# Kernel tuning notes

Measured on AMD Instinct MI355X. Metric: run time of the kernel, lower is better.

Reference implementation:

```python
import jax, jax.numpy as jnp
import numpy as np

B, S, F = 4, 2048, 512
H, DH, OUT = 8, 64, 512  # attention_dim=512 -> head_dim=64
NEG_SLOPE = 0.01


def setup_inputs() -> dict:
    key = jax.random.key(0)
    ks = jax.random.split(key, 9)
    sc_in = 1.0 / np.sqrt(F)
    sc_hd = 1.0 / np.sqrt(H * DH)
    return {
        "x": jax.random.normal(ks[0], (B, S, F), dtype=jnp.float32),
        "Wq": jax.random.normal(ks[1], (F, H, DH), dtype=jnp.float32) * sc_in,
        "bq": jnp.zeros((H, DH), dtype=jnp.float32),
        "Wk": jax.random.normal(ks[2], (F, H, DH), dtype=jnp.float32) * sc_in,
        "bk": jnp.zeros((H, DH), dtype=jnp.float32),
        "Wv": jax.random.normal(ks[3], (F, H, DH), dtype=jnp.float32) * sc_in,
        "bv": jnp.zeros((H, DH), dtype=jnp.float32),
        "Wo": jax.random.normal(ks[4], (H, DH, OUT), dtype=jnp.float32) * sc_hd,
        "bo": jnp.zeros((OUT,), dtype=jnp.float32),
    }


def reference(x, Wq, bq, Wk, bk, Wv, bv, Wo, bo):
    # QKV projections: DenseGeneral(axis=-1, features=(H, DH)) -> [B, S, H, DH]
    q = jnp.einsum('bsf,fhd->bshd', x, Wq) + bq
    k = jnp.einsum('bsf,fhd->bshd', x, Wk) + bk
    v = jnp.einsum('bsf,fhd->bshd', x, Wv) + bv

    # Pairwise squared L2: l2[b,h,i,j] = ||q[b,i,h]-k[b,j,h]||^2
    q2 = jnp.sum(q * q, axis=-1)              # [B, S, H]
    k2 = jnp.sum(k * k, axis=-1)              # [B, S, H]
    qk = jnp.einsum('bihd,bjhd->bhij', q, k)  # [B, H, S, S]
    l2 = (q2.transpose(0, 2, 1)[:, :, :, None]
          + k2.transpose(0, 2, 1)[:, :, None, :]
          - 2.0 * qk)

    # softmax over key axis j, then weights.T @ value (note the transpose:
    # output token index is j, summed over query index i, as in the original)
    w = jax.nn.softmax(-l2, axis=-1)                  # [B, H, Si, Sj]
    attn = jnp.einsum('bhij,bihd->bjhd', w, v)        # [B, S, H, DH]

    # out DenseGeneral contracting (H, DH)
    out = jnp.einsum('bshd,hdo->bso', attn, Wo) + bo
    return jnp.where(out >= 0, out, NEG_SLOPE * out)
```

## Files before the change

### kernel.cpp

```cpp
#include <hip/hip_runtime.h>


typedef __attribute__((ext_vector_type(8))) short bf16x8;
typedef __attribute__((ext_vector_type(4))) float f32x4;
typedef __attribute__((ext_vector_type(4))) unsigned short u16x4;

#define MFMA16 __builtin_amdgcn_mfma_f32_16x16x32_bf16
#define LOG2E 1.4426950408889634f
#define TWO_LOG2E 2.8853900817779268f

__device__ inline unsigned short f2bf(float f) {
  unsigned int u = __float_as_uint(f);
  unsigned int r = 0x7fffu + ((u >> 16) & 1u);
  return (unsigned short)((u + r) >> 16);
}
__device__ inline float bf2f(unsigned short h) {
  return __uint_as_float(((unsigned int)h) << 16);
}
__device__ inline float fexp2(float x) { return __builtin_amdgcn_exp2f(x); }

__device__ inline void gl_lds16(const unsigned short* g, unsigned short* lds) {
  __builtin_amdgcn_global_load_lds(
      (const __attribute__((address_space(1))) unsigned int*)g,
      (__attribute__((address_space(3))) unsigned int*)lds, 16, 0, 0);
}

#define NXB4 (8192*512/4)

__global__ __launch_bounds__(256) void prep(
    const float* __restrict__ x, const float* __restrict__ bq,
    const float* __restrict__ bk, const float* __restrict__ bv,
    unsigned short* __restrict__ xb, float* __restrict__ biasp) {
  int i = blockIdx.x * blockDim.x + threadIdx.x;
  if (i < NXB4) {
    f32x4 v = ((const f32x4*)x)[i];
    u16x4 o;
    o.x = f2bf(v.x); o.y = f2bf(v.y); o.z = f2bf(v.z); o.w = f2bf(v.w);
    ((u16x4*)xb)[i] = o;
    return;
  }
  i -= NXB4;
  if (i < 1536) {
    biasp[i] = (i < 512) ? bq[i] : (i < 1024) ? bk[i - 512] : bv[i - 1024];
  }
}

__global__ __launch_bounds__(256) void packW(
    const float* __restrict__ Wq, const float* __restrict__ Wk,
    const float* __restrict__ Wv, const float* __restrict__ Wo,
    unsigned short* __restrict__ wqkvT, unsigned short* __restrict__ woT) {
  const int m = blockIdx.x >> 6;
  const int n0 = ((blockIdx.x >> 3) & 7) * 64;
  const int f0 = (blockIdx.x & 7) * 64;
  const float* W = (m == 0) ? Wq : (m == 1) ? Wk : (m == 2) ? Wv : Wo;
  __shared__ float tile[64][65];
  const int t = threadIdx.x;
  const int c = t & 63, r4 = t >> 6;
#pragma unroll
  for (int k = 0; k < 16; ++k) {
    const int r = r4 + k * 4;
    tile[r][c] = W[(size_t)(f0 + r) * 512 + n0 + c];
  }
  __syncthreads();
#pragma unroll
  for (int k = 0; k < 16; ++k) {
    const int n_idx = r4 + k * 4, f_idx = c;
    const unsigned short v = f2bf(tile[f_idx][n_idx]);
    if (m < 3)
      wqkvT[(size_t)(m * 512 + n0 + n_idx) * 512 + f0 + f_idx] = v;
    else
      woT[(size_t)(n0 + n_idx) * 512 + f0 + f_idx] = v;
  }
}

template<int MODE>
__global__ __launch_bounds__(256) void gemm_bt(
    const unsigned short* __restrict__ A, const unsigned short* __restrict__ Bt,
    const float* __restrict__ bias,
    unsigned short* __restrict__ o_q, unsigned short* __restrict__ o_k,
    unsigned short* __restrict__ o_v, float* __restrict__ o_f,
    float* __restrict__ k2l_g, int K) {
  const int lid = blockIdx.x + blockIdx.y * gridDim.x;
  const int tot = gridDim.x * gridDim.y;
  const int lid2 = (lid & 7) * (tot >> 3) + (lid >> 3);
  const int m0 = (lid2 / gridDim.x) * 128;
  const int n0 = (lid2 % gridDim.x) * 128;
  const int tid = threadIdx.x;
  const int w = tid >> 6, l = tid & 63, lg = l >> 4, ll = l & 15;
  const int wr = w >> 1, wc = w & 1;
  __shared__ unsigned short a_lds[2][128 * 32];
  __shared__ unsigned short b_lds[2][128 * 32];
  f32x4 acc[4][4] = {};
  const int nkt = K >> 5;
  const int cb0 = w * 64, cb1 = 256 + w * 64;
  const int cc0 = cb0 + l, cc1 = cb1 + l;
  const int ar0 = cc0 >> 2, ac0 = cc0 & 3, ar1 = cc1 >> 2, ac1 = cc1 & 3;
  gl_lds16(A + (size_t)(m0 + ar0) * K + ac0 * 8, &a_lds[0][cb0 * 8]);
  gl_lds16(A + (size_t)(m0 + ar1) * K + ac1 * 8, &a_lds[0][cb1 * 8]);
  gl_lds16(Bt + (size_t)(n0 + ar0) * K + ac0 * 8, &b_lds[0][cb0 * 8]);
  gl_lds16(Bt + (size_t)(n0 + ar1) * K + ac1 * 8, &b_lds[0][cb1 * 8]);
  __syncthreads();
  for (int kt = 0; kt < nkt; ++kt) {
    const int slot = kt & 1;
    if (kt + 1 < nkt) {
      const int k1 = (kt + 1) * 32;
      gl_lds16(A + (size_t)(m0 + ar0) * K + k1 + ac0 * 8, &a_lds[slot ^ 1][cb0 * 8]);
      gl_lds16(A + (size_t)(m0 + ar1) * K + k1 + ac1 * 8, &a_lds[slot ^ 1][cb1 * 8]);
      gl_lds16(Bt + (size_t)(n0 + ar0) * K + k1 + ac0 * 8, &b_lds[slot ^ 1][cb0 * 8]);
      gl_lds16(Bt + (size_t)(n0 + ar1) * K + k1 + ac1 * 8, &b_lds[slot ^ 1][cb1 * 8]);
    }
    bf16x8 af[4], bfr[4];
#pragma unroll
    for (int mi = 0; mi < 4; ++mi)
      af[mi] = *(const bf16x8*)(&a_lds[slot][(wr * 64 + mi * 16 + ll) * 32 + lg * 8]);
#pragma unroll
    for (int ni = 0; ni < 4; ++ni)
      bfr[ni] = *(const bf16x8*)(&b_lds[slot][(wc * 64 + ni * 16 + ll) * 32 + lg * 8]);
#pragma unroll
    for (int mi = 0; mi < 4; ++mi)
#pragma unroll
      for (int ni = 0; ni < 4; ++ni)
        acc[mi][ni] = MFMA16(af[mi], bfr[ni], acc[mi][ni], 0, 0, 0);
    __syncthreads();
  }
#pragma unroll
  for (int mi = 0; mi < 4; ++mi)
#pragma unroll
    for (int ni = 0; ni < 4; ++ni) {
      const int col = n0 + wc * 64 + ni * 16 + ll;
      const float bb = bias[col];
#pragma unroll
      for (int r = 0; r < 4; ++r) {
        const int row = m0 + wr * 64 + mi * 16 + lg * 4 + r;
        float v = acc[mi][ni][r] + bb;
        if (MODE == 0) {
          const int which = col >> 9, h = (col >> 6) & 7, d = col & 63;
          const int b = row >> 11, s = row & 2047;
          if (which == 0) v *= TWO_LOG2E;
          const size_t idx = ((size_t)((b * 8 + h) * 2048 + s)) * 64 + d;
          (which == 0 ? o_q : which == 1 ? o_k : o_v)[idx] = f2bf(v);
        } else {
          v = v >= 0.f ? v : 0.01f * v;
          o_f[(size_t)row * 512 + col] = v;
        }
      }
    }
  if (MODE == 0 && n0 >= 512 && n0 < 1024) {
    const int h = ((n0 + wc * 64) >> 6) & 7;
#pragma unroll
    for (int mi = 0; mi < 4; ++mi)
#pragma unroll
      for (int r = 0; r < 4; ++r) {
        float s2 = 0.f;
#pragma unroll
        for (int ni = 0; ni < 4; ++ni) {
          const int col = n0 + wc * 64 + ni * 16 + ll;
          const float v = acc[mi][ni][r] + bias[col];
          s2 += v * v;
        }
#pragma unroll
        for (int m = 1; m < 16; m <<= 1) s2 += __shfl_xor(s2, m);
        if (ll == 0) {
          const int row = m0 + wr * 64 + mi * 16 + lg * 4 + r;
          const int b = row >> 11, s = row & 2047;
          k2l_g[(size_t)(b * 8 + h) * 2048 + s] = LOG2E * s2;
        }
      }
  }
}

__global__ __launch_bounds__(256) void transpose_v(const unsigned short* __restrict__ v_g,
                                                   const float* __restrict__ invl_g,
                                                   unsigned short* __restrict__ vt_g) {
  const int bh = blockIdx.x >> 5, st = blockIdx.x & 31;
  const int s0 = st * 64;
  __shared__ unsigned short tile[64][72];
  const int t = threadIdx.x;
  {
    const int sl = t >> 2, cg = t & 3;
    const float sc = invl_g[bh * 2048 + s0 + sl];
    const unsigned short* src = v_g + ((size_t)(bh * 2048 + s0 + sl)) * 64 + cg * 16;
    bf16x8 v0 = *(const bf16x8*)(src);
    bf16x8 v1 = *(const bf16x8*)(src + 8);
#pragma unroll
    for (int e = 0; e < 8; ++e) tile[sl][cg * 16 + e] = f2bf(sc * bf2f((unsigned short)v0[e]));
#pragma unroll
    for (int e = 0; e < 8; ++e) tile[sl][cg * 16 + 8 + e] = f2bf(sc * bf2f((unsigned short)v1[e]));
  }
  __syncthreads();
  {
    const int dl = t >> 2, sg = t & 3;
    bf16x8 o0, o1;
#pragma unroll
    for (int e = 0; e < 8; ++e) o0[e] = (short)tile[sg * 16 + e][dl];
#pragma unroll
    for (int e = 0; e < 8; ++e) o1[e] = (short)tile[sg * 16 + 8 + e][dl];
    unsigned short* dst = vt_g + ((size_t)(bh * 64 + dl)) * 2048 + s0 + sg * 16;
    *(bf16x8*)dst = o0;
    *(bf16x8*)(dst + 8) = o1;
  }
}

__global__ __launch_bounds__(256) void pass1(const unsigned short* __restrict__ q_g,
                                             const unsigned short* __restrict__ k_g,
                                             const float* __restrict__ k2l_g,
                                             float* __restrict__ invl_g) {
  const int bx = blockIdx.x;
  const int bh = (bx & 7) * 4 + ((bx >> 3) >> 4);
  const int ib = (bx >> 3) & 15;
  const int i0 = ib * 128;
  const int tid = threadIdx.x, w = tid >> 6, l = tid & 63, lg = l >> 4, ll = l & 15;
  __shared__ unsigned short k_lds[2][64 * 64];
  __shared__ float k2_lds[2][64];
  const unsigned short* k_bh = k_g + (size_t)bh * 2048 * 64;
  const unsigned short* qrow = q_g + ((size_t)(bh * 2048 + i0 + w * 32 + ll)) * 64;
  const bf16x8 qa00 = *(const bf16x8*)(qrow + lg * 8);
  const bf16x8 qa01 = *(const bf16x8*)(qrow + 32 + lg * 8);
  const bf16x8 qa10 = *(const bf16x8*)(qrow + 1024 + lg * 8);
  const bf16x8 qa11 = *(const bf16x8*)(qrow + 1024 + 32 + lg * 8);
  float lrun0[4] = {0.f, 0.f, 0.f, 0.f};
  float lrun1[4] = {0.f, 0.f, 0.f, 0.f};
  const int cb0 = w * 64, cb1 = 256 + w * 64;
  const int cc0 = cb0 + l, cc1 = cb1 + l;
  const int r0_ = cc0 >> 3, c0_ = cc0 & 7, r1_ = cc1 >> 3, c1_ = cc1 & 7;
  const int so0 = (c0_ ^ (r0_ & 7)) * 8;
  const int so1 = (c1_ ^ (r1_ & 7)) * 8;
  gl_lds16(k_bh + (size_t)r0_ * 64 + so0, &k_lds[0][cb0 * 8]);
  gl_lds16(k_bh + (size_t)r1_ * 64 + so1, &k_lds[0][cb1 * 8]);
  if (tid < 64) k2_lds[0][tid] = k2l_g[bh * 2048 + tid];
  __syncthreads();
  for (int jt = 0; jt < 32; ++jt) {
    const int slot = jt & 1;
    if (jt + 1 < 32) {
      const int j1 = (jt + 1) * 64;
      gl_lds16(k_bh + (size_t)(j1 + r0_) * 64 + so0, &k_lds[slot ^ 1][cb0 * 8]);
      gl_lds16(k_bh + (size_t)(j1 + r1_) * 64 + so1, &k_lds[slot ^ 1][cb1 * 8]);
      if (tid < 64) k2_lds[slot ^ 1][tid] = k2l_g[bh * 2048 + j1 + tid];
    }
#pragma unroll
    for (int nf = 0; nf < 4; ++nf) {
      const int jr = nf * 16 + ll;
      const unsigned short* kb = &k_lds[slot][jr * 64];
      const int sw = jr & 7;
      bf16x8 b0 = *(const bf16x8*)(kb + ((lg ^ sw) * 8));
      bf16x8 b1 = *(const bf16x8*)(kb + (((4 + lg) ^ sw) * 8));
      f32x4 sa0 = {};
      sa0 = MFMA16(qa00, b0, sa0, 0, 0, 0);
      sa0 = MFMA16(qa01, b1, sa0, 0, 0, 0);
      f32x4 sa1 = {};
      sa1 = MFMA16(qa10, b0, sa1, 0, 0, 0);
      sa1 = MFMA16(qa11, b1, sa1, 0, 0, 0);
      const float k2v = k2_lds[slot][jr];
      lrun0[0] += fexp2(sa0[0] - k2v);
      lrun0[1] += fexp2(sa0[1] - k2v);
      lrun0[2] += fexp2(sa0[2] - k2v);
      lrun0[3] += fexp2(sa0[3] - k2v);
      lrun1[0] += fexp2(sa1[0] - k2v);
      lrun1[1] += fexp2(sa1[1] - k2v);
      lrun1[2] += fexp2(sa1[2] - k2v);
      lrun1[3] += fexp2(sa1[3] - k2v);
    }
    __syncthreads();
  }
#pragma unroll
  for (int r = 0; r < 4; ++r) {
    float t0 = lrun0[r], t1 = lrun1[r];
#pragma unroll
    for (int m = 1; m < 16; m <<= 1) { t0 += __shfl_xor(t0, m); t1 += __shfl_xor(t1, m); }
    if (ll == 0) {
      invl_g[bh * 2048 + i0 + w * 32 + lg * 4 + r] = 1.f / t0;
      invl_g[bh * 2048 + i0 + w * 32 + 16 + lg * 4 + r] = 1.f / t1;
    }
  }
}

__global__ __launch_bounds__(256) void pass2(const unsigned short* __restrict__ q_g,
                                             const unsigned short* __restrict__ k_g,
                                             const unsigned short* __restrict__ vt_g,
                                             const float* __restrict__ k2l_g,
                                             unsigned short* __restrict__ part0,
                                             unsigned short* __restrict__ part1,
                                             unsigned short* __restrict__ part2) {
  const int bx = blockIdx.x;
  const int bh = (bx & 7) * 4 + ((bx >> 3) >> 4);
  const int jb = (bx >> 3) & 15;
  const int by = blockIdx.y;
  const int j0 = jb * 128;
  const int it0 = by * 11;
  const int it_end = (by == 2) ? 32 : it0 + 11;
  const int tid = threadIdx.x, w = tid >> 6, l = tid & 63, lg = l >> 4, ll = l & 15;
  __shared__ unsigned short q_lds[2][64 * 64];
  __shared__ unsigned short vt_lds[2][64 * 64];
  __shared__ unsigned short p_lds[128 * 64];
  const unsigned short* q_base = q_g + (size_t)bh * 2048 * 64;
  const unsigned short* vt_base = vt_g + (size_t)bh * 64 * 2048;
  const unsigned short* krow = k_g + ((size_t)(bh * 2048 + j0 + w * 32 + ll)) * 64;
  const bf16x8 ka00 = *(const bf16x8*)(krow + lg * 8);
  const bf16x8 ka01 = *(const bf16x8*)(krow + 32 + lg * 8);
  const bf16x8 ka10 = *(const bf16x8*)(krow + 1024 + lg * 8);
  const bf16x8 ka11 = *(const bf16x8*)(krow + 1024 + 32 + lg * 8);
  float k2v0[4], k2v1[4];
#pragma unroll
  for (int r = 0; r < 4; ++r) {
    k2v0[r] = k2l_g[bh * 2048 + j0 + w * 32 + lg * 4 + r];
    k2v1[r] = k2l_g[bh * 2048 + j0 + w * 32 + 16 + lg * 4 + r];
  }
  f32x4 oacc0[4] = {};
  f32x4 oacc1[4] = {};
  const int pslot = it0 & 1;
#pragma unroll
  for (int c = 0; c < 2; ++c) {
    const int cc_base = c * 256 + w * 64;
    const int cc = cc_base + l;
    const int row = cc >> 3, cl = cc & 7;
    const int csw = (cl ^ (row & 7)) * 8;
    gl_lds16(q_base + (size_t)(it0 * 64 + row) * 64 + csw, &q_lds[pslot][cc_base * 8]);
    gl_lds16(vt_base + (size_t)row * 2048 + it0 * 64 + csw, &vt_lds[pslot][cc_base * 8]);
  }
  __syncthreads();
  for (int it = it0; it < it_end; ++it) {
    const int slot = it & 1;
    if (it + 1 < it_end) {
      const int i1 = (it + 1) * 64;
#pragma unroll
      for (int c = 0; c < 2; ++c) {
        const int cc_base = c * 256 + w * 64;
        const int cc = cc_base + l;
        const int row = cc >> 3, cl = cc & 7;
        const int csw = (cl ^ (row & 7)) * 8;
        gl_lds16(q_base + (size_t)(i1 + row) * 64 + csw, &q_lds[slot ^ 1][cc_base * 8]);
        gl_lds16(vt_base + (size_t)row * 2048 + i1 + csw, &vt_lds[slot ^ 1][cc_base * 8]);
      }
    }
#pragma unroll
    for (int nf = 0; nf < 4; ++nf) {
      const int ir = nf * 16 + ll;
      const unsigned short* qb = &q_lds[slot][ir * 64];
      const int sw = ir & 7;
      bf16x8 b0 = *(const bf16x8*)(qb + ((lg ^ sw) * 8));
      bf16x8 b1 = *(const bf16x8*)(qb + (((4 + lg) ^ sw) * 8));
      f32x4 sa0 = {};
      sa0 = MFMA16(ka00, b0, sa0, 0, 0, 0);
      sa0 = MFMA16(ka01, b1, sa0, 0, 0, 0);
      f32x4 sa1 = {};
      sa1 = MFMA16(ka10, b0, sa1, 0, 0, 0);
      sa1 = MFMA16(ka11, b1, sa1, 0, 0, 0);
#pragma unroll
      for (int r = 0; r < 4; ++r) {
        const float p0 = fexp2(sa0[r] - k2v0[r]);
        const float p1 = fexp2(sa1[r] - k2v1[r]);
        const int ja = w * 32 + lg * 4 + r;
        const int jb2 = ja + 16;
        p_lds[ja * 64 + (ir ^ ((ja & 7) << 3))] =
            (unsigned short)(__float_as_uint(p0) >> 16);
        p_lds[jb2 * 64 + (ir ^ ((jb2 & 7) << 3))] =
            (unsigned short)(__float_as_uint(p1) >> 16);
      }
    }
    {
      const int jr0 = w * 32 + ll;
      const int jr1 = jr0 + 16;
      const int swp = ll & 7;
      const unsigned short* pb0 = p_lds + jr0 * 64;
      const unsigned short* pb1 = p_lds + jr1 * 64;
      bf16x8 pa00 = *(const bf16x8*)(pb0 + ((lg ^ swp) * 8));
      bf16x8 pa01 = *(const bf16x8*)(pb0 + (((4 + lg) ^ swp) * 8));
      bf16x8 pa10 = *(const bf16x8*)(pb1 + ((lg ^ swp) * 8));
      bf16x8 pa11 = *(const bf16x8*)(pb1 + (((4 + lg) ^ swp) * 8));
#pragma unroll
      for (int nf = 0; nf < 4; ++nf) {
        const int dr = nf * 16 + ll;
        const unsigned short* vb = &vt_lds[slot][dr * 64];
        const int sw = dr & 7;
        bf16x8 v0 = *(const bf16x8*)(vb + ((lg ^ sw) * 8));
        bf16x8 v1 = *(const bf16x8*)(vb + (((4 + lg) ^ sw) * 8));
        oacc0[nf] = MFMA16(pa00, v0, oacc0[nf], 0, 0, 0);
        oacc0[nf] = MFMA16(pa01, v1, oacc0[nf], 0, 0, 0);
        oacc1[nf] = MFMA16(pa10, v0, oacc1[nf], 0, 0, 0);
        oacc1[nf] = MFMA16(pa11, v1, oacc1[nf], 0, 0, 0);
      }
    }
    __syncthreads();
  }
  unsigned short* po = (by == 0) ? part0 : (by == 1) ? part1 : part2;
  const int b = bh >> 3, h2 = bh & 7;
#pragma unroll
  for (int nf = 0; nf < 4; ++nf) {
    const int d = nf * 16 + ll;
#pragma unroll
    for (int r = 0; r < 4; ++r) {
      const int j = j0 + w * 32 + lg * 4 + r;
      po[((size_t)(b * 2048 + j)) * 512 + h2 * 64 + d] = f2bf(oacc0[nf][r]);
      po[((size_t)(b * 2048 + j + 16)) * 512 + h2 * 64 + d] = f2bf(oacc1[nf][r]);
    }
  }
}

__global__ __launch_bounds__(256) void combine3(unsigned short* __restrict__ p0,
                                                const unsigned short* __restrict__ p1,
                                                const unsigned short* __restrict__ p2) {
  const int i = blockIdx.x * blockDim.x + threadIdx.x;
  bf16x8 a = ((const bf16x8*)p0)[i];
  bf16x8 b = ((const bf16x8*)p1)[i];
  bf16x8 c = ((const bf16x8*)p2)[i];
  bf16x8 o;
#pragma unroll
  for (int e = 0; e < 8; ++e)
    o[e] = (short)f2bf(bf2f((unsigned short)a[e]) + bf2f((unsigned short)b[e]) +
                       bf2f((unsigned short)c[e]));
  ((bf16x8*)p0)[i] = o;
}

extern "C" void kernel_launch(void* const* d_in, const int* in_sizes, int n_in,
                              void* d_out, int out_size, void* d_ws, size_t ws_size,
                              hipStream_t stream) {
  const float* x  = (const float*)d_in[0];
  const float* Wq = (const float*)d_in[1];
  const float* bq = (const float*)d_in[2];
  const float* Wk = (const float*)d_in[3];
  const float* bk = (const float*)d_in[4];
  const float* Wv = (const float*)d_in[5];
  const float* bv = (const float*)d_in[6];
  const float* Wo = (const float*)d_in[7];
  const float* bo = (const float*)d_in[8];
  float* out = (float*)d_out;
  char* ws = (char*)d_ws;

  unsigned short* xb    = (unsigned short*)(ws);
  unsigned short* wqkvT = (unsigned short*)(ws + 8388608);
  unsigned short* woT   = (unsigned short*)(ws + 9961472);
  float*          biasp = (float*)         (ws + 10485760);
  unsigned short* q_g   = (unsigned short*)(ws + 10493952);
  unsigned short* k_g   = (unsigned short*)(ws + 18882560);
  unsigned short* v_g   = (unsigned short*)(ws + 27271168);
  unsigned short* vt_g  = (unsigned short*)(ws + 35659776);
  float*          k2_g  = (float*)         (ws + 44048384);
  float*          invl_g= (float*)         (ws + 44310528);
  unsigned short* attnb = (unsigned short*)(ws + 44572672);
  if (ws_size < (size_t)52961280) return;

  prep<<<4102, 256, 0, stream>>>(x, bq, bk, bv, xb, biasp);
  packW<<<256, 256, 0, stream>>>(Wq, Wk, Wv, Wo, wqkvT, woT);
  gemm_bt<0><<<dim3(12, 64), 256, 0, stream>>>(xb, wqkvT, biasp, q_g, k_g, v_g, nullptr, k2_g, 512);
  pass1<<<512, 256, 0, stream>>>(q_g, k_g, k2_g, invl_g);
  transpose_v<<<1024, 256, 0, stream>>>(v_g, invl_g, vt_g);
  pass2<<<dim3(512, 3), 256, 0, stream>>>(q_g, k_g, vt_g, k2_g, attnb, xb, v_g);
  combine3<<<2048, 256, 0, stream>>>(attnb, xb, v_g);
  gemm_bt<1><<<dim3(4, 64), 256, 0, stream>>>(attnb, woT, bo, nullptr, nullptr, nullptr, out, nullptr, 512);
}
```

Before: 154.5 us.

## Merge prep and weight packing kernels; load V fragments directly from global in pass2

Fuses the x-to-bf16 conversion and the weight transpose/pack into one launch by dispatching on block index, which removes one kernel launch. In pass2 the V^T tile no longer goes through a double-buffered LDS copy; each lane loads its MFMA B-operand fragments straight from global memory into registers every iteration. This cuts LDS usage and LDS traffic, which may improve occupancy, but it exposes global-load latency inside the loop with no explicit prefetch. The merged prep kernel also makes every block allocate the 64x65 float tile in shared memory, even the conversion blocks that never use it.

```diff
diff --git a/kernel.cpp b/kernel.cpp
--- a/kernel.cpp
+++ b/kernel.cpp
@@ -26,34 +26,36 @@
 }
 
 #define NXB4 (8192*512/4)
-
-__global__ __launch_bounds__(256) void prep(
-    const float* __restrict__ x, const float* __restrict__ bq,
+#define PREP_BLOCKS 4102
+
+__global__ __launch_bounds__(256) void prep_all(
+    const float* __restrict__ x, const float* __restrict__ Wq,
+    const float* __restrict__ Wk, const float* __restrict__ Wv,
+    const float* __restrict__ Wo, const float* __restrict__ bq,
     const float* __restrict__ bk, const float* __restrict__ bv,
-    unsigned short* __restrict__ xb, float* __restrict__ biasp) {
-  int i = blockIdx.x * blockDim.x + threadIdx.x;
-  if (i < NXB4) {
-    f32x4 v = ((const f32x4*)x)[i];
-    u16x4 o;
-    o.x = f2bf(v.x); o.y = f2bf(v.y); o.z = f2bf(v.z); o.w = f2bf(v.w);
-    ((u16x4*)xb)[i] = o;
+    unsigned short* __restrict__ xb, unsigned short* __restrict__ wqkvT,
+    unsigned short* __restrict__ woT, float* __restrict__ biasp) {
+  __shared__ float tile[64][65];
+  if (blockIdx.x < PREP_BLOCKS) {
+    int i = blockIdx.x * blockDim.x + threadIdx.x;
+    if (i < NXB4) {
+      f32x4 v = ((const f32x4*)x)[i];
+      u16x4 o;
+      o.x = f2bf(v.x); o.y = f2bf(v.y); o.z = f2bf(v.z); o.w = f2bf(v.w);
+      ((u16x4*)xb)[i] = o;
+      return;
+    }
+    i -= NXB4;
+    if (i < 1536) {
+      biasp[i] = (i < 512) ? bq[i] : (i < 1024) ? bk[i - 512] : bv[i - 1024];
+    }
     return;
   }
-  i -= NXB4;
-  if (i < 1536) {
-    biasp[i] = (i < 512) ? bq[i] : (i < 1024) ? bk[i - 512] : bv[i - 1024];
-  }
-}
-
-__global__ __launch_bounds__(256) void packW(
-    const float* __restrict__ Wq, const float* __restrict__ Wk,
-    const float* __restrict__ Wv, const float* __restrict__ Wo,
-    unsigned short* __restrict__ wqkvT, unsigned short* __restrict__ woT) {
-  const int m = blockIdx.x >> 6;
-  const int n0 = ((blockIdx.x >> 3) & 7) * 64;
-  const int f0 = (blockIdx.x & 7) * 64;
+  const int bid = blockIdx.x - PREP_BLOCKS;
+  const int m = bid >> 6;
+  const int n0 = ((bid >> 3) & 7) * 64;
+  const int f0 = (bid & 7) * 64;
   const float* W = (m == 0) ? Wq : (m == 1) ? Wk : (m == 2) ? Wv : Wo;
-  __shared__ float tile[64][65];
   const int t = threadIdx.x;
   const int c = t & 63, r4 = t >> 6;
 #pragma unroll
@@ -290,7 +292,6 @@
   const int it_end = (by == 2) ? 32 : it0 + 11;
   const int tid = threadIdx.x, w = tid >> 6, l = tid & 63, lg = l >> 4, ll = l & 15;
   __shared__ unsigned short q_lds[2][64 * 64];
-  __shared__ unsigned short vt_lds[2][64 * 64];
   __shared__ unsigned short p_lds[128 * 64];
   const unsigned short* q_base = q_g + (size_t)bh * 2048 * 64;
   const unsigned short* vt_base = vt_g + (size_t)bh * 64 * 2048;
@@ -305,6 +306,7 @@
     k2v0[r] = k2l_g[bh * 2048 + j0 + w * 32 + lg * 4 + r];
     k2v1[r] = k2l_g[bh * 2048 + j0 + w * 32 + 16 + lg * 4 + r];
   }
+  const unsigned short* vrow_base = vt_base + (size_t)ll * 2048 + lg * 8;
   f32x4 oacc0[4] = {};
   f32x4 oacc1[4] = {};
   const int pslot = it0 & 1;
@@ -315,7 +317,6 @@
     const int row = cc >> 3, cl = cc & 7;
     const int csw = (cl ^ (row & 7)) * 8;
     gl_lds16(q_base + (size_t)(it0 * 64 + row) * 64 + csw, &q_lds[pslot][cc_base * 8]);
-    gl_lds16(vt_base + (size_t)row * 2048 + it0 * 64 + csw, &vt_lds[pslot][cc_base * 8]);
   }
   __syncthreads();
   for (int it = it0; it < it_end; ++it) {
@@ -329,8 +330,14 @@
         const int row = cc >> 3, cl = cc & 7;
         const int csw = (cl ^ (row & 7)) * 8;
         gl_lds16(q_base + (size_t)(i1 + row) * 64 + csw, &q_lds[slot ^ 1][cc_base * 8]);
-        gl_lds16(vt_base + (size_t)row * 2048 + i1 + csw, &vt_lds[slot ^ 1][cc_base * 8]);
       }
+    }
+    bf16x8 vfr[4][2];
+#pragma unroll
+    for (int nf = 0; nf < 4; ++nf) {
+      const unsigned short* vr = vrow_base + (size_t)(nf * 16) * 2048 + it * 64;
+      vfr[nf][0] = *(const bf16x8*)(vr);
+      vfr[nf][1] = *(const bf16x8*)(vr + 32);
     }
 #pragma unroll
     for (int nf = 0; nf < 4; ++nf) {
@@ -369,15 +376,10 @@
       bf16x8 pa11 = *(const bf16x8*)(pb1 + (((4 + lg) ^ swp) * 8));
 #pragma unroll
       for (int nf = 0; nf < 4; ++nf) {
-        const int dr = nf * 16 + ll;
-        const unsigned short* vb = &vt_lds[slot][dr * 64];
-        const int sw = dr & 7;
-        bf16x8 v0 = *(const bf16x8*)(vb + ((lg ^ sw) * 8));
-        bf16x8 v1 = *(const bf16x8*)(vb + (((4 + lg) ^ sw) * 8));
-        oacc0[nf] = MFMA16(pa00, v0, oacc0[nf], 0, 0, 0);
-        oacc0[nf] = MFMA16(pa01, v1, oacc0[nf], 0, 0, 0);
-        oacc1[nf] = MFMA16(pa10, v0, oacc1[nf], 0, 0, 0);
-        oacc1[nf] = MFMA16(pa11, v1, oacc1[nf], 0, 0, 0);
+        oacc0[nf] = MFMA16(pa00, vfr[nf][0], oacc0[nf], 0, 0, 0);
+        oacc0[nf] = MFMA16(pa01, vfr[nf][1], oacc0[nf], 0, 0, 0);
+        oacc1[nf] = MFMA16(pa10, vfr[nf][0], oacc1[nf], 0, 0, 0);
+        oacc1[nf] = MFMA16(pa11, vfr[nf][1], oacc1[nf], 0, 0, 0);
       }
     }
     __syncthreads();
@@ -439,8 +441,7 @@
   unsigned short* attnb = (unsigned short*)(ws + 44572672);
   if (ws_size < (size_t)52961280) return;
 
-  prep<<<4102, 256, 0, stream>>>(x, bq, bk, bv, xb, biasp);
-  packW<<<256, 256, 0, stream>>>(Wq, Wk, Wv, Wo, wqkvT, woT);
+  prep_all<<<4358, 256, 0, stream>>>(x, Wq, Wk, Wv, Wo, bq, bk, bv, xb, wqkvT, woT, biasp);
   gemm_bt<0><<<dim3(12, 64), 256, 0, stream>>>(xb, wqkvT, biasp, q_g, k_g, v_g, nullptr, k2_g, 512);
   pass1<<<512, 256, 0, stream>>>(q_g, k_g, k2_g, invl_g);
   transpose_v<<<1024, 256, 0, stream>>>(v_g, invl_g, vt_g);
```

Measured after the change: 172.9 us. 11.9% more time.
